# Kernel tuning notes

Hardware: AMD Instinct MI355X
Metric: run time of the kernel (lower is better)

Reference implementation:

```python
import jax, jax.numpy as jnp
import numpy as np

N = 100000      # number of graph nodes (len(graph.x))
E = 3200000     # number of edges (avg degree 32)
IN = 128        # latent input_size


def setup_inputs() -> dict:
    key = jax.random.key(0)
    ks = jax.random.split(key, 16)
    s = 0.02
    return {
        "x": jax.random.normal(ks[0], (1, IN), jnp.float32),
        "edge_index": jax.random.randint(ks[1], (2, E), 0, N, jnp.int64),
        "W1": jax.random.normal(ks[2], (IN, 256), jnp.float32) * s,
        "b1": jnp.zeros((256,), jnp.float32),
        "W2": jax.random.normal(ks[3], (256, 512), jnp.float32) * s,
        "b2": jnp.zeros((512,), jnp.float32),
        "W3": jax.random.normal(ks[4], (512, N * 4), jnp.float32) * s,
        "b3": jnp.zeros((N * 4,), jnp.float32),
        "Wg1": jax.random.normal(ks[5], (4, 2), jnp.float32) * 0.5,
        "bg1": jnp.zeros((2,), jnp.float32),
        "Wg2": jax.random.normal(ks[6], (2, 1), jnp.float32) * 0.5,
        "bg2": jnp.zeros((1,), jnp.float32),
    }


def _gcn_conv(h, W, b, src, dst):
    # PyG GCNConv: linear transform, add self-loops, symmetric normalization
    # deg computed on dst (col) index after self-loops, norm = d^-1/2[src]*d^-1/2[dst]
    m = h @ W                                   # [N, out]
    deg = jnp.zeros((N,), m.dtype).at[dst].add(1.0) + 1.0  # +1 for self-loop
    dinv = jax.lax.rsqrt(deg)
    norm = dinv[src] * dinv[dst]                # [E]
    agg = jnp.zeros((N, m.shape[1]), m.dtype).at[dst].add(m[src] * norm[:, None])
    agg = agg + m * (1.0 / deg)[:, None]        # self-loop: norm = deg^-1
    return agg + b


def reference(x, edge_index, W1, b1, W2, b2, W3, b3, Wg1, bg1, Wg2, bg2):
    src, dst = edge_index[0], edge_index[1]
    h = jax.nn.relu(x @ W1 + b1)
    h = jax.nn.relu(h @ W2 + b2)
    h = jax.nn.relu(h @ W3 + b3)
    h = h.reshape(N, 4)
    h = jax.nn.relu(_gcn_conv(h, Wg1, bg1, src, dst))
    h = _gcn_conv(h, Wg2, bg2, src, dst)
    return jax.nn.sigmoid(h).reshape(-1)
```

## Files before the change

### kernel.cpp

```cpp
#include <hip/hip_runtime.h>
#include <math.h>

#define NN 100000
#define NE 3200000

__global__ __launch_bounds__(64) void mlp12_kernel(
        const float* __restrict__ x,
        const float* __restrict__ W1, const float* __restrict__ b1,
        const float* __restrict__ W2, const float* __restrict__ b2,
        float* __restrict__ h2g) {
    __shared__ float xs[128];
    __shared__ float h1s[256];
    int t = threadIdx.x;
    xs[t] = x[t];
    xs[t + 64] = x[t + 64];
    __syncthreads();
    for (int cc = 0; cc < 4; ++cc) {
        int c = t + cc * 64;
        float acc = b1[c];
        for (int k = 0; k < 128; ++k) acc = fmaf(xs[k], W1[k * 256 + c], acc);
        h1s[c] = fmaxf(acc, 0.0f);
    }
    __syncthreads();
    int c2 = blockIdx.x * 64 + t;
    float acc = b2[c2];
    for (int k = 0; k < 256; ++k) acc = fmaf(h1s[k], W2[k * 512 + c2], acc);
    h2g[c2] = fmaxf(acc, 0.0f);
}

__global__ __launch_bounds__(256) void big_layer_kernel(
        const float* __restrict__ h2, const float* __restrict__ W3,
        const float* __restrict__ b3, const float* __restrict__ Wg1,
        float* __restrict__ m1) {
    __shared__ float h2s[512];
    __shared__ float ps[4][64][4];
    int t = threadIdx.x;
    h2s[t] = h2[t];
    h2s[t + 256] = h2[t + 256];
    __syncthreads();
    int ks = t >> 6;
    int ns = t & 63;
    int node = blockIdx.x * 64 + ns;
    float a0 = 0.f, a1 = 0.f, a2 = 0.f, a3 = 0.f;
    if (node < NN) {
        int k0 = ks * 128;
        const float4* p =
            reinterpret_cast<const float4*>(W3 + (size_t)k0 * 400000 + 4 * (size_t)node);
        for (int it = 0; it < 128; ++it) {
            float4 w = p[(size_t)it * 100000];
            float hv = h2s[k0 + it];
            a0 = fmaf(hv, w.x, a0);
            a1 = fmaf(hv, w.y, a1);
            a2 = fmaf(hv, w.z, a2);
            a3 = fmaf(hv, w.w, a3);
        }
    }
    ps[ks][ns][0] = a0; ps[ks][ns][1] = a1; ps[ks][ns][2] = a2; ps[ks][ns][3] = a3;
    __syncthreads();
    if (ks == 0 && node < NN) {
        float t0 = ps[0][ns][0] + ps[1][ns][0] + ps[2][ns][0] + ps[3][ns][0];
        float t1 = ps[0][ns][1] + ps[1][ns][1] + ps[2][ns][1] + ps[3][ns][1];
        float t2 = ps[0][ns][2] + ps[1][ns][2] + ps[2][ns][2] + ps[3][ns][2];
        float t3 = ps[0][ns][3] + ps[1][ns][3] + ps[2][ns][3] + ps[3][ns][3];
        const float4 bb = *reinterpret_cast<const float4*>(b3 + 4 * (size_t)node);
        t0 = fmaxf(t0 + bb.x, 0.0f);
        t1 = fmaxf(t1 + bb.y, 0.0f);
        t2 = fmaxf(t2 + bb.z, 0.0f);
        t3 = fmaxf(t3 + bb.w, 0.0f);
        float m0 = t0 * Wg1[0] + t1 * Wg1[2] + t2 * Wg1[4] + t3 * Wg1[6];
        float mv = t0 * Wg1[1] + t1 * Wg1[3] + t2 * Wg1[5] + t3 * Wg1[7];
        m1[2 * node]     = m0;
        m1[2 * node + 1] = mv;
    }
}

__global__ __launch_bounds__(256) void deg_kernel(const int* __restrict__ dst,
                                                  float* __restrict__ deg) {
    int e = blockIdx.x * 256 + threadIdx.x;
    if (e < NE) atomicAdd(&deg[dst[e]], 1.0f);
}

__global__ __launch_bounds__(256) void node1_kernel(const float* __restrict__ deg,
                                                    const float* __restrict__ m1,
                                                    float* __restrict__ dinv,
                                                    float* __restrict__ agg1) {
    int i = blockIdx.x * 256 + threadIdx.x;
    if (i < NN) {
        float d = deg[i] + 1.0f;
        dinv[i] = rsqrtf(d);
        float inv = 1.0f / d;
        agg1[2 * i]     = m1[2 * i] * inv;
        agg1[2 * i + 1] = m1[2 * i + 1] * inv;
    }
}

__global__ __launch_bounds__(256) void edge1_kernel(const int* __restrict__ src,
                                                    const int* __restrict__ dst,
                                                    const float* __restrict__ dinv,
                                                    const float* __restrict__ m1,
                                                    float* __restrict__ agg1) {
    int e = blockIdx.x * 256 + threadIdx.x;
    if (e < NE) {
        int s = src[e], d = dst[e];
        float n = dinv[s] * dinv[d];
        atomicAdd(&agg1[2 * d],     m1[2 * s] * n);
        atomicAdd(&agg1[2 * d + 1], m1[2 * s + 1] * n);
    }
}

__global__ __launch_bounds__(256) void node2_kernel(const float* __restrict__ agg1,
                                                    const float* __restrict__ bg1,
                                                    const float* __restrict__ Wg2,
                                                    const float* __restrict__ deg,
                                                    float* __restrict__ m2,
                                                    float* __restrict__ agg2) {
    int i = blockIdx.x * 256 + threadIdx.x;
    if (i < NN) {
        float g0 = fmaxf(agg1[2 * i] + bg1[0], 0.0f);
        float g1 = fmaxf(agg1[2 * i + 1] + bg1[1], 0.0f);
        float mv = g0 * Wg2[0] + g1 * Wg2[1];
        m2[i] = mv;
        float d = deg[i] + 1.0f;
        agg2[i] = mv / d;
    }
}

__global__ __launch_bounds__(256) void edge2_kernel(const int* __restrict__ src,
                                                    const int* __restrict__ dst,
                                                    const float* __restrict__ dinv,
                                                    const float* __restrict__ m2,
                                                    float* __restrict__ agg2) {
    int e = blockIdx.x * 256 + threadIdx.x;
    if (e < NE) {
        int s = src[e], d = dst[e];
        atomicAdd(&agg2[d], m2[s] * dinv[s] * dinv[d]);
    }
}

__global__ __launch_bounds__(256) void sigmoid_kernel(const float* __restrict__ agg2,
                                                      const float* __restrict__ bg2,
                                                      float* __restrict__ out) {
    int i = blockIdx.x * 256 + threadIdx.x;
    if (i < NN) {
        float v = agg2[i] + bg2[0];
        out[i] = 1.0f / (1.0f + __expf(-v));
    }
}

extern "C" void kernel_launch(void* const* d_in, const int* in_sizes, int n_in,
                              void* d_out, int out_size, void* d_ws, size_t ws_size,
                              hipStream_t stream) {
    const float* x   = (const float*)d_in[0];
    const int*   ei  = (const int*)d_in[1];
    const float* W1  = (const float*)d_in[2];
    const float* b1  = (const float*)d_in[3];
    const float* W2  = (const float*)d_in[4];
    const float* b2  = (const float*)d_in[5];
    const float* W3  = (const float*)d_in[6];
    const float* b3  = (const float*)d_in[7];
    const float* Wg1 = (const float*)d_in[8];
    const float* bg1 = (const float*)d_in[9];
    const float* Wg2 = (const float*)d_in[10];
    const float* bg2 = (const float*)d_in[11];
    float* out = (float*)d_out;

    const int* src = ei;
    const int* dst = ei + NE;

    float* ws   = (float*)d_ws;
    float* h2   = ws;
    float* m1   = h2 + 512;
    float* deg  = m1 + 2 * NN;
    float* dinv = deg + NN;
    float* agg1 = dinv + NN;
    float* m2   = agg1 + 2 * NN;
    float* agg2 = m2 + NN;

    hipMemsetAsync(deg, 0, NN * sizeof(float), stream);

    mlp12_kernel<<<8, 64, 0, stream>>>(x, W1, b1, W2, b2, h2);
    deg_kernel<<<(NE + 255) / 256, 256, 0, stream>>>(dst, deg);
    big_layer_kernel<<<(NN + 63) / 64, 256, 0, stream>>>(h2, W3, b3, Wg1, m1);
    node1_kernel<<<(NN + 255) / 256, 256, 0, stream>>>(deg, m1, dinv, agg1);
    edge1_kernel<<<(NE + 255) / 256, 256, 0, stream>>>(src, dst, dinv, m1, agg1);
    node2_kernel<<<(NN + 255) / 256, 256, 0, stream>>>(agg1, bg1, Wg2, deg, m2, agg2);
    edge2_kernel<<<(NE + 255) / 256, 256, 0, stream>>>(src, dst, dinv, m2, agg2);
    sigmoid_kernel<<<(NN + 255) / 256, 256, 0, stream>>>(agg2, bg2, out);
}
```

Before: 1.746 ms.

## Fuse degree count into big layer, vectorize edge kernels, cache edge norms

Folds the degree atomic counting into the big GEMV kernel, which now handles 128 nodes per block with two float4 loads per row, so the atomics overlap the W3 stream and one launch goes away. The edge kernels now process four edges per thread with int4 index loads. The first edge pass stores the per-edge norm so the second pass reads it in order instead of gathering dinv twice. The trade-off is an extra 12.8MB norm buffer write and read, plus atomic contention inside the memory-bound GEMV.

```diff
diff --git a/kernel.cpp b/kernel.cpp
--- a/kernel.cpp
+++ b/kernel.cpp
@@ -3,6 +3,7 @@
 
 #define NN 100000
 #define NE 3200000
+#define BL_BLOCKS 782
 
 __global__ __launch_bounds__(64) void mlp12_kernel(
         const float* __restrict__ x,
@@ -31,53 +32,55 @@
 __global__ __launch_bounds__(256) void big_layer_kernel(
         const float* __restrict__ h2, const float* __restrict__ W3,
         const float* __restrict__ b3, const float* __restrict__ Wg1,
+        const int* __restrict__ dst, float* __restrict__ deg,
         float* __restrict__ m1) {
     __shared__ float h2s[512];
-    __shared__ float ps[4][64][4];
+    __shared__ float ps[4][128][4];
     int t = threadIdx.x;
     h2s[t] = h2[t];
     h2s[t + 256] = h2[t + 256];
     __syncthreads();
     int ks = t >> 6;
-    int ns = t & 63;
-    int node = blockIdx.x * 64 + ns;
-    float a0 = 0.f, a1 = 0.f, a2 = 0.f, a3 = 0.f;
-    if (node < NN) {
-        int k0 = ks * 128;
-        const float4* p =
-            reinterpret_cast<const float4*>(W3 + (size_t)k0 * 400000 + 4 * (size_t)node);
+    int lane = t & 63;
+    int nb = blockIdx.x * 128;
+    int n0 = nb + 2 * lane;
+    float a0=0.f,a1=0.f,a2=0.f,a3=0.f,a4=0.f,a5=0.f,a6=0.f,a7=0.f;
+    if (n0 < NN) {
+        const float* q = W3 + (size_t)(ks * 128) * 400000 + 4 * (size_t)n0;
+        #pragma unroll 8
         for (int it = 0; it < 128; ++it) {
-            float4 w = p[(size_t)it * 100000];
-            float hv = h2s[k0 + it];
-            a0 = fmaf(hv, w.x, a0);
-            a1 = fmaf(hv, w.y, a1);
-            a2 = fmaf(hv, w.z, a2);
-            a3 = fmaf(hv, w.w, a3);
+            float4 w0 = *reinterpret_cast<const float4*>(q);
+            float4 w1 = *reinterpret_cast<const float4*>(q + 4);
+            float hv = h2s[ks * 128 + it];
+            a0 = fmaf(hv, w0.x, a0); a1 = fmaf(hv, w0.y, a1);
+            a2 = fmaf(hv, w0.z, a2); a3 = fmaf(hv, w0.w, a3);
+            a4 = fmaf(hv, w1.x, a4); a5 = fmaf(hv, w1.y, a5);
+            a6 = fmaf(hv, w1.z, a6); a7 = fmaf(hv, w1.w, a7);
+            q += 400000;
         }
     }
-    ps[ks][ns][0] = a0; ps[ks][ns][1] = a1; ps[ks][ns][2] = a2; ps[ks][ns][3] = a3;
-    __syncthreads();
-    if (ks == 0 && node < NN) {
-        float t0 = ps[0][ns][0] + ps[1][ns][0] + ps[2][ns][0] + ps[3][ns][0];
-        float t1 = ps[0][ns][1] + ps[1][ns][1] + ps[2][ns][1] + ps[3][ns][1];
-        float t2 = ps[0][ns][2] + ps[1][ns][2] + ps[2][ns][2] + ps[3][ns][2];
-        float t3 = ps[0][ns][3] + ps[1][ns][3] + ps[2][ns][3] + ps[3][ns][3];
-        const float4 bb = *reinterpret_cast<const float4*>(b3 + 4 * (size_t)node);
-        t0 = fmaxf(t0 + bb.x, 0.0f);
-        t1 = fmaxf(t1 + bb.y, 0.0f);
-        t2 = fmaxf(t2 + bb.z, 0.0f);
-        t3 = fmaxf(t3 + bb.w, 0.0f);
-        float m0 = t0 * Wg1[0] + t1 * Wg1[2] + t2 * Wg1[4] + t3 * Wg1[6];
-        float mv = t0 * Wg1[1] + t1 * Wg1[3] + t2 * Wg1[5] + t3 * Wg1[7];
-        m1[2 * node]     = m0;
-        m1[2 * node + 1] = mv;
-    }
-}
-
-__global__ __launch_bounds__(256) void deg_kernel(const int* __restrict__ dst,
-                                                  float* __restrict__ deg) {
-    int e = blockIdx.x * 256 + threadIdx.x;
-    if (e < NE) atomicAdd(&deg[dst[e]], 1.0f);
+    *reinterpret_cast<float4*>(&ps[ks][2 * lane][0])     = make_float4(a0, a1, a2, a3);
+    *reinterpret_cast<float4*>(&ps[ks][2 * lane + 1][0]) = make_float4(a4, a5, a6, a7);
+    for (int e = blockIdx.x * 256 + t; e < NE; e += BL_BLOCKS * 256)
+        atomicAdd(&deg[dst[e]], 1.0f);
+    __syncthreads();
+    if (t < 128) {
+        int node = nb + t;
+        if (node < NN) {
+            float4 s0 = *reinterpret_cast<float4*>(&ps[0][t][0]);
+            float4 s1 = *reinterpret_cast<float4*>(&ps[1][t][0]);
+            float4 s2 = *reinterpret_cast<float4*>(&ps[2][t][0]);
+            float4 s3 = *reinterpret_cast<float4*>(&ps[3][t][0]);
+            float4 bb = *reinterpret_cast<const float4*>(b3 + 4 * (size_t)node);
+            float t0 = fmaxf(s0.x + s1.x + s2.x + s3.x + bb.x, 0.0f);
+            float t1 = fmaxf(s0.y + s1.y + s2.y + s3.y + bb.y, 0.0f);
+            float t2 = fmaxf(s0.z + s1.z + s2.z + s3.z + bb.z, 0.0f);
+            float t3 = fmaxf(s0.w + s1.w + s2.w + s3.w + bb.w, 0.0f);
+            float m0 = t0 * Wg1[0] + t1 * Wg1[2] + t2 * Wg1[4] + t3 * Wg1[6];
+            float mv = t0 * Wg1[1] + t1 * Wg1[3] + t2 * Wg1[5] + t3 * Wg1[7];
+            reinterpret_cast<float2*>(m1)[node] = make_float2(m0, mv);
+        }
+    }
 }
 
 __global__ __launch_bounds__(256) void node1_kernel(const float* __restrict__ deg,
@@ -89,8 +92,8 @@
         float d = deg[i] + 1.0f;
         dinv[i] = rsqrtf(d);
         float inv = 1.0f / d;
-        agg1[2 * i]     = m1[2 * i] * inv;
-        agg1[2 * i + 1] = m1[2 * i + 1] * inv;
+        float2 mv = reinterpret_cast<const float2*>(m1)[i];
+        reinterpret_cast<float2*>(agg1)[i] = make_float2(mv.x * inv, mv.y * inv);
     }
 }
 
@@ -98,14 +101,30 @@
                                                     const int* __restrict__ dst,
                                                     const float* __restrict__ dinv,
                                                     const float* __restrict__ m1,
+                                                    float* __restrict__ norm,
                                                     float* __restrict__ agg1) {
-    int e = blockIdx.x * 256 + threadIdx.x;
-    if (e < NE) {
-        int s = src[e], d = dst[e];
-        float n = dinv[s] * dinv[d];
-        atomicAdd(&agg1[2 * d],     m1[2 * s] * n);
-        atomicAdd(&agg1[2 * d + 1], m1[2 * s + 1] * n);
-    }
+    int i = blockIdx.x * 256 + threadIdx.x;
+    if (i * 4 >= NE) return;
+    int4 s4 = reinterpret_cast<const int4*>(src)[i];
+    int4 d4 = reinterpret_cast<const int4*>(dst)[i];
+    const float2* m1f2 = reinterpret_cast<const float2*>(m1);
+    float n0 = dinv[s4.x] * dinv[d4.x];
+    float n1 = dinv[s4.y] * dinv[d4.y];
+    float n2 = dinv[s4.z] * dinv[d4.z];
+    float n3 = dinv[s4.w] * dinv[d4.w];
+    float2 v0 = m1f2[s4.x];
+    float2 v1 = m1f2[s4.y];
+    float2 v2 = m1f2[s4.z];
+    float2 v3 = m1f2[s4.w];
+    reinterpret_cast<float4*>(norm)[i] = make_float4(n0, n1, n2, n3);
+    atomicAdd(&agg1[2 * d4.x],     v0.x * n0);
+    atomicAdd(&agg1[2 * d4.x + 1], v0.y * n0);
+    atomicAdd(&agg1[2 * d4.y],     v1.x * n1);
+    atomicAdd(&agg1[2 * d4.y + 1], v1.y * n1);
+    atomicAdd(&agg1[2 * d4.z],     v2.x * n2);
+    atomicAdd(&agg1[2 * d4.z + 1], v2.y * n2);
+    atomicAdd(&agg1[2 * d4.w],     v3.x * n3);
+    atomicAdd(&agg1[2 * d4.w + 1], v3.y * n3);
 }
 
 __global__ __launch_bounds__(256) void node2_kernel(const float* __restrict__ agg1,
@@ -116,25 +135,29 @@
                                                     float* __restrict__ agg2) {
     int i = blockIdx.x * 256 + threadIdx.x;
     if (i < NN) {
-        float g0 = fmaxf(agg1[2 * i] + bg1[0], 0.0f);
-        float g1 = fmaxf(agg1[2 * i + 1] + bg1[1], 0.0f);
+        float2 av = reinterpret_cast<const float2*>(agg1)[i];
+        float g0 = fmaxf(av.x + bg1[0], 0.0f);
+        float g1 = fmaxf(av.y + bg1[1], 0.0f);
         float mv = g0 * Wg2[0] + g1 * Wg2[1];
         m2[i] = mv;
-        float d = deg[i] + 1.0f;
-        agg2[i] = mv / d;
+        agg2[i] = mv / (deg[i] + 1.0f);
     }
 }
 
 __global__ __launch_bounds__(256) void edge2_kernel(const int* __restrict__ src,
                                                     const int* __restrict__ dst,
-                                                    const float* __restrict__ dinv,
+                                                    const float* __restrict__ norm,
                                                     const float* __restrict__ m2,
                                                     float* __restrict__ agg2) {
-    int e = blockIdx.x * 256 + threadIdx.x;
-    if (e < NE) {
-        int s = src[e], d = dst[e];
-        atomicAdd(&agg2[d], m2[s] * dinv[s] * dinv[d]);
-    }
+    int i = blockIdx.x * 256 + threadIdx.x;
+    if (i * 4 >= NE) return;
+    int4 s4 = reinterpret_cast<const int4*>(src)[i];
+    int4 d4 = reinterpret_cast<const int4*>(dst)[i];
+    float4 nv = reinterpret_cast<const float4*>(norm)[i];
+    atomicAdd(&agg2[d4.x], m2[s4.x] * nv.x);
+    atomicAdd(&agg2[d4.y], m2[s4.y] * nv.y);
+    atomicAdd(&agg2[d4.z], m2[s4.z] * nv.z);
+    atomicAdd(&agg2[d4.w], m2[s4.w] * nv.w);
 }
 
 __global__ __launch_bounds__(256) void sigmoid_kernel(const float* __restrict__ agg2,
@@ -175,15 +198,15 @@
     float* agg1 = dinv + NN;
     float* m2   = agg1 + 2 * NN;
     float* agg2 = m2 + NN;
+    float* norm = agg2 + NN;
 
     hipMemsetAsync(deg, 0, NN * sizeof(float), stream);
 
     mlp12_kernel<<<8, 64, 0, stream>>>(x, W1, b1, W2, b2, h2);
-    deg_kernel<<<(NE + 255) / 256, 256, 0, stream>>>(dst, deg);
-    big_layer_kernel<<<(NN + 63) / 64, 256, 0, stream>>>(h2, W3, b3, Wg1, m1);
+    big_layer_kernel<<<BL_BLOCKS, 256, 0, stream>>>(h2, W3, b3, Wg1, dst, deg, m1);
     node1_kernel<<<(NN + 255) / 256, 256, 0, stream>>>(deg, m1, dinv, agg1);
-    edge1_kernel<<<(NE + 255) / 256, 256, 0, stream>>>(src, dst, dinv, m1, agg1);
+    edge1_kernel<<<(NE / 4 + 255) / 256, 256, 0, stream>>>(src, dst, dinv, m1, norm, agg1);
     node2_kernel<<<(NN + 255) / 256, 256, 0, stream>>>(agg1, bg1, Wg2, deg, m2, agg2);
-    edge2_kernel<<<(NE + 255) / 256, 256, 0, stream>>>(src, dst, dinv, m2, agg2);
+    edge2_kernel<<<(NE / 4 + 255) / 256, 256, 0, stream>>>(src, dst, norm, m2, agg2);
     sigmoid_kernel<<<(NN + 255) / 256, 256, 0, stream>>>(agg2, bg2, out);
 }
```

Measured after the change: 1.733 ms. About the same (-0.8%).
